# Performance work log

Measured on AMD Instinct MI355X. Metric: run time of the kernel, lower is better.

## Reference

```python
import jax, jax.numpy as jnp
import numpy as np

N_NODES = 100000
N_EDGES = 1600000
DIM = 64
NUM_HEADS = 4
HEAD_DIM = DIM // NUM_HEADS
QK_SCALE = HEAD_DIM ** -0.5
EPS = 1e-16  # matches torch_geometric softmax denominator eps


def setup_inputs() -> dict:
    key = jax.random.key(0)
    k1, k2, k3 = jax.random.split(key, 3)
    x = jax.random.normal(k1, (N_NODES, DIM), dtype=jnp.float32)
    W_qkv = jax.random.normal(k2, (DIM, 3 * DIM), dtype=jnp.float32) * (DIM ** -0.5)
    b_qkv = jnp.zeros((3 * DIM,), dtype=jnp.float32)
    edge_index = jax.random.randint(k3, (2, N_EDGES), 0, N_NODES, dtype=jnp.int64)
    return {"x": x, "W_qkv": W_qkv, "b_qkv": b_qkv, "edge_index": edge_index}


def reference(x, W_qkv, b_qkv, edge_index):
    N = x.shape[0]
    E = edge_index.shape[1]
    # qkv projection: (N, 3, H, d)
    qkv = (x @ W_qkv + b_qkv).reshape(N, 3, NUM_HEADS, HEAD_DIM)
    s = edge_index[0]  # query (source) node per edge
    t = edge_index[1]  # key/value (target) node per edge
    q = qkv[s, 0] * QK_SCALE  # (E, H, d)
    k = qkv[t, 1]             # (E, H, d)
    v = qkv[t, 2]             # (E, H, d)
    compat = jnp.einsum('ehd,ehd->eh', q, k)  # (E, H)
    # segment softmax keyed by source node (numerically stable)
    m = jax.ops.segment_max(compat, s, num_segments=N)          # (N, H)
    ex = jnp.exp(compat - m[s])                                  # (E, H)
    den = jax.ops.segment_sum(ex, s, num_segments=N)             # (N, H)
    attn = ex / (den[s] + EPS)                                   # (E, H)
    # weighted values, flatten heads, scatter-sum back to source nodes
    msg = (v * attn[..., None]).reshape(E, DIM)                  # (E, dim)
    out = jax.ops.segment_sum(msg, s, num_segments=N)            # (N, dim)
    return out
```

## Files before the change

### kernel.cpp

```cpp
#include <hip/hip_runtime.h>

constexpr int N_NODES = 100000;
constexpr int N_EDGES = 1600000;
constexpr int DIM = 64;
constexpr float QK_SCALE = 0.25f;
constexpr float LOG2E = 1.4426950408889634f;
constexpr float EPS = 1e-16f;

constexpr int NBK = (N_NODES + 255) / 256;
constexpr int BCAP = 8192;
constexpr int SC_CHUNK = 4096;
constexpr int SC_BLOCKS = (N_EDGES + SC_CHUNK - 1) / SC_CHUNK;
constexpr int QK_BLOCKS = (N_NODES + 127) / 128;
constexpr int TPAD = 200;

typedef __attribute__((ext_vector_type(8))) short short8;
typedef __attribute__((ext_vector_type(4))) float f32x4;
typedef _Float16 h2 __attribute__((ext_vector_type(2)));

__device__ __forceinline__ unsigned short f32_to_bf16_rne(float f) {
    unsigned int u = __float_as_uint(f);
    u += 0x7fffu + ((u >> 16) & 1u);
    return (unsigned short)(u >> 16);
}
__device__ __forceinline__ h2 as_h2(unsigned int u) { return __builtin_bit_cast(h2, u); }

#if defined(__has_builtin)
#if __has_builtin(__builtin_amdgcn_fdot2)
#define HAVE_FDOT2 1
#endif
#endif
__device__ __forceinline__ float fdot2_acc(h2 a, h2 b, float c) {
#ifdef HAVE_FDOT2
    return __builtin_amdgcn_fdot2(a, b, c, false);
#else
    return fmaf((float)a.x, (float)b.x, fmaf((float)a.y, (float)b.y, c));
#endif
}

__device__ __forceinline__ float qsum4(float p) {
    int a = __builtin_amdgcn_update_dpp(0, __float_as_int(p), 0xB1, 0xF, 0xF, true);
    p += __int_as_float(a);
    int c = __builtin_amdgcn_update_dpp(0, __float_as_int(p), 0x4E, 0xF, 0xF, true);
    p += __int_as_float(c);
    return p;
}

__device__ __forceinline__ int orig_col(int jp) {
    if (jp < 64) return jp;
    const int p = jp - 64;
    const int chunk = p >> 3, w = p & 7;
    return (w < 4) ? (64 + chunk * 4 + w) : (128 + chunk * 4 + (w - 4));
}

__global__ __launch_bounds__(192) void prep_w(const float* __restrict__ W,
                                              const float* __restrict__ b,
                                              unsigned short* __restrict__ Wbt,
                                              float* __restrict__ bb,
                                              int* __restrict__ bcnt) {
    const int jp = threadIdx.x;
    const int k = blockIdx.x;
    const int oc = orig_col(jp);
    const float sc = (jp < 64) ? QK_SCALE * LOG2E : 1.f;
    Wbt[jp * DIM + k] = f32_to_bf16_rne(W[k * 192 + oc] * sc);
    if (k == 0) {
        bb[jp] = b[oc] * sc;
        for (int i = jp; i < NBK; i += 192) bcnt[i] = 0;
    }
}

__global__ __launch_bounds__(512) void proj_scatter(const float* __restrict__ x,
                                                    const unsigned short* __restrict__ Wbt,
                                                    const float* __restrict__ bb,
                                                    unsigned short* __restrict__ qkv_t,
                                                    const int* __restrict__ ei,
                                                    int* __restrict__ bcnt,
                                                    unsigned int* __restrict__ bbuf) {
    __shared__ __align__(16) char smem[128 * TPAD * 2];

    if (blockIdx.x < SC_BLOCKS) {
        unsigned int* stage = (unsigned int*)smem;
        int* h     = (int*)(smem + SC_CHUNK * 4);
        int* lofs  = h + NBK;
        int* gbase = lofs + NBK;
        int* wsum  = gbase + NBK;

        const int tid = threadIdx.x;
        const int lane = tid & 63;
        const int wid = tid >> 6;
        const int e0 = blockIdx.x * SC_CHUNK;
        const int n = min(SC_CHUNK, N_EDGES - e0);
        const int n4 = n >> 2;

        for (int i = tid; i < NBK; i += 512) h[i] = 0;
        __syncthreads();

        const int4* s4p = (const int4*)(ei + e0);
        for (int i = tid; i < n4; i += 512) {
            const int4 s4 = s4p[i];
            atomicAdd(&h[s4.x >> 8], 1);
            atomicAdd(&h[s4.y >> 8], 1);
            atomicAdd(&h[s4.z >> 8], 1);
            atomicAdd(&h[s4.w >> 8], 1);
        }
        __syncthreads();

        const int v = (tid < NBK) ? h[tid] : 0;
        int inc = v;
        #pragma unroll
        for (int d = 1; d < 64; d <<= 1) {
            int u = __shfl_up(inc, d);
            if (lane >= d) inc += u;
        }
        if (lane == 63) wsum[wid] = inc;
        __syncthreads();
        int woff = 0;
        for (int w = 0; w < wid; ++w) woff += wsum[w];
        if (tid < NBK) lofs[tid] = woff + inc - v;
        if (tid < NBK) gbase[tid] = (v > 0) ? atomicAdd(&bcnt[tid], v) : 0;
        __syncthreads();

        for (int i = tid; i < NBK; i += 512) h[i] = 0;
        __syncthreads();

        const int4* t4p = (const int4*)(ei + N_EDGES + e0);
        for (int i = tid; i < n4; i += 512) {
            const int4 s4 = s4p[i];
            const int4 t4 = t4p[i];
            #pragma unroll
            for (int k = 0; k < 4; ++k) {
                const int s = (k == 0) ? s4.x : (k == 1) ? s4.y : (k == 2) ? s4.z : s4.w;
                const int t = (k == 0) ? t4.x : (k == 1) ? t4.y : (k == 2) ? t4.z : t4.w;
                const int bk = s >> 8;
                const int c = atomicAdd(&h[bk], 1);
                stage[lofs[bk] + c] = (unsigned int)t | ((unsigned int)(s & 255) << 17);
            }
        }
        __syncthreads();

        for (int bk = wid; bk < NBK; bk += 8) {
            const int cnt = h[bk];
            const int lo = lofs[bk];
            unsigned int* dst = bbuf + (size_t)bk * BCAP + gbase[bk];
            for (int i = lane; i < cnt; i += 64) dst[i] = stage[lo + i];
        }
    } else {
        unsigned short* tile = (unsigned short*)smem;

        const int tid = threadIdx.x;
        const int lane = tid & 63;
        const int wid = tid >> 6;
        const int nb0 = (blockIdx.x - SC_BLOCKS) * 128;
        const int n0 = nb0 + wid * 16;
        const bool active = n0 < N_NODES;
        const int row = lane & 15;
        const int kg = lane >> 4;

        if (active) {
            const int nidx = min(n0 + row, N_NODES - 1);
            const float* xr = x + (size_t)nidx * DIM + kg * 8;
            short8 a0, a1;
            {
                const float4 u0 = *(const float4*)(xr);
                const float4 u1 = *(const float4*)(xr + 4);
                const float4 u2 = *(const float4*)(xr + 32);
                const float4 u3 = *(const float4*)(xr + 36);
                a0[0] = (short)f32_to_bf16_rne(u0.x); a0[1] = (short)f32_to_bf16_rne(u0.y);
                a0[2] = (short)f32_to_bf16_rne(u0.z); a0[3] = (short)f32_to_bf16_rne(u0.w);
                a0[4] = (short)f32_to_bf16_rne(u1.x); a0[5] = (short)f32_to_bf16_rne(u1.y);
                a0[6] = (short)f32_to_bf16_rne(u1.z); a0[7] = (short)f32_to_bf16_rne(u1.w);
                a1[0] = (short)f32_to_bf16_rne(u2.x); a1[1] = (short)f32_to_bf16_rne(u2.y);
                a1[2] = (short)f32_to_bf16_rne(u2.z); a1[3] = (short)f32_to_bf16_rne(u2.w);
                a1[4] = (short)f32_to_bf16_rne(u3.x); a1[5] = (short)f32_to_bf16_rne(u3.y);
                a1[6] = (short)f32_to_bf16_rne(u3.z); a1[7] = (short)f32_to_bf16_rne(u3.w);
            }

            #pragma unroll
            for (int ct = 0; ct < 12; ++ct) {
                const int c0 = ct * 16;
                const float bias = bb[c0 + row];
                f32x4 acc = {bias, bias, bias, bias};
                const short8 b0 = *(const short8*)(Wbt + (c0 + row) * DIM + kg * 8);
                const short8 b1 = *(const short8*)(Wbt + (c0 + row) * DIM + kg * 8 + 32);
                acc = __builtin_amdgcn_mfma_f32_16x16x32_bf16(a0, b0, acc, 0, 0, 0);
                acc = __builtin_amdgcn_mfma_f32_16x16x32_bf16(a1, b1, acc, 0, 0, 0);

                const int colg = c0 + row;
                #pragma unroll
                for (int r = 0; r < 4; ++r) {
                    const _Float16 hv = (_Float16)acc[r];
                    tile[(wid * 16 + kg * 4 + r) * TPAD + colg] =
                        __builtin_bit_cast(unsigned short, hv);
                }
            }
        }
        __syncthreads();

        for (int i = tid; i < 128 * 24; i += 512) {
            const int r = i / 24, c = i % 24;
            if (nb0 + r < N_NODES) {
                const uint4 val = *(const uint4*)(tile + r * TPAD + c * 8);
                ((uint4*)(qkv_t + (size_t)(nb0 + r) * 192))[c] = val;
            }
        }
    }
}

__global__ __launch_bounds__(512) void csr_build(const int* __restrict__ bcnt,
                                                 const unsigned int* __restrict__ bbuf,
                                                 int* __restrict__ deg,
                                                 int* __restrict__ off,
                                                 int* __restrict__ sorted_t) {
    __shared__ int h[256];
    __shared__ int lofs[256];
    __shared__ int wsum[8];
    __shared__ int sBase;

    const int tid = threadIdx.x;
    const int lane = tid & 63;
    const int wid = tid >> 6;
    const int bk = blockIdx.x;
    const int n = bcnt[bk];

    int pre = 0;
    for (int i = tid; i < bk; i += 512) pre += bcnt[i];
    #pragma unroll
    for (int d = 1; d < 64; d <<= 1) pre += __shfl_xor(pre, d);
    if (lane == 0) wsum[wid] = pre;
    if (tid < 256) h[tid] = 0;
    __syncthreads();
    if (tid == 0) {
        int s = 0;
        #pragma unroll
        for (int w = 0; w < 8; ++w) s += wsum[w];
        sBase = s;
    }
    __syncthreads();

    const unsigned int* p = bbuf + (size_t)bk * BCAP;
    for (int i = tid; i < n; i += 512)
        atomicAdd(&h[p[i] >> 17], 1);
    __syncthreads();

    int v = 0, inc = 0;
    if (tid < 256) {
        v = h[tid];
        inc = v;
        #pragma unroll
        for (int d = 1; d < 64; d <<= 1) {
            int u = __shfl_up(inc, d);
            if (lane >= d) inc += u;
        }
        if (lane == 63) wsum[wid] = inc;
    }
    __syncthreads();
    if (tid < 256) {
        int woff = 0;
        for (int w = 0; w < wid; ++w) woff += wsum[w];
        const int exc = woff + inc - v;
        lofs[tid] = exc;
        const int node = bk * 256 + tid;
        if (node < N_NODES) { deg[node] = v; off[node] = sBase + exc; }
    }
    __syncthreads();

    if (tid < 256) h[tid] = 0;
    __syncthreads();
    int* dstbase = sorted_t + sBase;
    for (int i = tid; i < n; i += 512) {
        const unsigned int e = p[i];
        const int s8 = e >> 17;
        const int c = atomicAdd(&h[s8], 1);
        dstbase[lofs[s8] + c] = (int)(e & 0x1FFFFu);
    }
}

__global__ __launch_bounds__(256) void node_pass(const unsigned short* __restrict__ qkv,
                                                 const int* __restrict__ off,
                                                 const int* __restrict__ deg,
                                                 const int* __restrict__ sorted_t,
                                                 float* __restrict__ out) {
    const int node = blockIdx.x * 4 + (threadIdx.x >> 6);
    const int lane = threadIdx.x & 63;
    if (node >= N_NODES) return;
    const int eg = lane >> 4;
    const int q16 = lane & 15;

    const int o = off[node];
    const int d = deg[node];

    const uint2 qu = *(const uint2*)(qkv + (size_t)node * 192 + q16 * 4);
    const h2 q01 = as_h2(qu.x), q23 = as_h2(qu.y);

    const float M0 = -1e30f, MASKV = -2e30f;
    float m = M0;
    float l = 0.f;
    float4 acc = make_float4(0.f, 0.f, 0.f, 0.f);

    for (int j = 0; j < d; j += 16) {
        const int b0 = j + eg * 4;
        const int dm = d - 1;
        const int t0 = sorted_t[o + min(b0,     dm)];
        const int t1 = sorted_t[o + min(b0 + 1, dm)];
        const int t2 = sorted_t[o + min(b0 + 2, dm)];
        const int t3 = sorted_t[o + min(b0 + 3, dm)];
        const uint4 A0 = *(const uint4*)(qkv + (size_t)t0 * 192 + 64 + q16 * 8);
        const uint4 A1 = *(const uint4*)(qkv + (size_t)t1 * 192 + 64 + q16 * 8);
        const uint4 A2 = *(const uint4*)(qkv + (size_t)t2 * 192 + 64 + q16 * 8);
        const uint4 A3 = *(const uint4*)(qkv + (size_t)t3 * 192 + 64 + q16 * 8);
        float p0 = fdot2_acc(as_h2(A0.y), q23, fdot2_acc(as_h2(A0.x), q01, 0.f));
        float p1 = fdot2_acc(as_h2(A1.y), q23, fdot2_acc(as_h2(A1.x), q01, 0.f));
        float p2 = fdot2_acc(as_h2(A2.y), q23, fdot2_acc(as_h2(A2.x), q01, 0.f));
        float p3 = fdot2_acc(as_h2(A3.y), q23, fdot2_acc(as_h2(A3.x), q01, 0.f));
        p0 = qsum4(p0); p1 = qsum4(p1); p2 = qsum4(p2); p3 = qsum4(p3);
        p0 = (b0     < d) ? p0 : MASKV;
        p1 = (b0 + 1 < d) ? p1 : MASKV;
        p2 = (b0 + 2 < d) ? p2 : MASKV;
        p3 = (b0 + 3 < d) ? p3 : MASKV;
        const float pm = fmaxf(fmaxf(p0, p1), fmaxf(p2, p3));
        if (__any(pm > m)) {
            const float nm = fmaxf(m, pm);
            const float sc = exp2f(m - nm);
            l *= sc;
            acc.x *= sc; acc.y *= sc; acc.z *= sc; acc.w *= sc;
            m = nm;
        }
        const float e0 = exp2f(p0 - m);
        const float e1 = exp2f(p1 - m);
        const float e2 = exp2f(p2 - m);
        const float e3 = exp2f(p3 - m);
        l += (e0 + e1) + (e2 + e3);
        const h2 va0 = as_h2(A0.z), vb0 = as_h2(A0.w);
        const h2 va1 = as_h2(A1.z), vb1 = as_h2(A1.w);
        const h2 va2 = as_h2(A2.z), vb2 = as_h2(A2.w);
        const h2 va3 = as_h2(A3.z), vb3 = as_h2(A3.w);
        acc.x = fmaf(e0, (float)va0.x, fmaf(e1, (float)va1.x,
                fmaf(e2, (float)va2.x, fmaf(e3, (float)va3.x, acc.x))));
        acc.y = fmaf(e0, (float)va0.y, fmaf(e1, (float)va1.y,
                fmaf(e2, (float)va2.y, fmaf(e3, (float)va3.y, acc.y))));
        acc.z = fmaf(e0, (float)vb0.x, fmaf(e1, (float)vb1.x,
                fmaf(e2, (float)vb2.x, fmaf(e3, (float)vb3.x, acc.z))));
        acc.w = fmaf(e0, (float)vb0.y, fmaf(e1, (float)vb1.y,
                fmaf(e2, (float)vb2.y, fmaf(e3, (float)vb3.y, acc.w))));
    }

    float M = fmaxf(m, __shfl_xor(m, 16));
    M = fmaxf(M, __shfl_xor(M, 32));
    const float s = exp2f(m - M);
    l *= s;
    acc.x *= s; acc.y *= s; acc.z *= s; acc.w *= s;

    l += __shfl_xor(l, 16);  l += __shfl_xor(l, 32);
    acc.x += __shfl_xor(acc.x, 16);  acc.x += __shfl_xor(acc.x, 32);
    acc.y += __shfl_xor(acc.y, 16);  acc.y += __shfl_xor(acc.y, 32);
    acc.z += __shfl_xor(acc.z, 16);  acc.z += __shfl_xor(acc.z, 32);
    acc.w += __shfl_xor(acc.w, 16);  acc.w += __shfl_xor(acc.w, 32);

    if (eg == 0) {
        const float inv = 1.f / (l + EPS);
        float4 r = make_float4(acc.x * inv, acc.y * inv, acc.z * inv, acc.w * inv);
        *(float4*)(out + (size_t)node * DIM + q16 * 4) = r;
    }
}

extern "C" void kernel_launch(void* const* d_in, const int* in_sizes, int n_in,
                              void* d_out, int out_size, void* d_ws, size_t ws_size,
                              hipStream_t stream) {
    const float* x = (const float*)d_in[0];
    const float* W = (const float*)d_in[1];
    const float* b = (const float*)d_in[2];
    const int*   ei = (const int*)d_in[3];
    float* out = (float*)d_out;

    unsigned short* qkv_t = (unsigned short*)d_ws;
    unsigned int* bbuf = (unsigned int*)(qkv_t + (size_t)N_NODES * 192);
    int* sorted_t = (int*)(bbuf + (size_t)NBK * BCAP);
    int* deg      = sorted_t + N_EDGES;
    int* off      = deg + N_NODES;
    int* bcnt     = off + N_NODES;
    unsigned short* Wbt = (unsigned short*)(bcnt + NBK);
    float* bb     = (float*)(Wbt + 192 * DIM);

    prep_w<<<64, 192, 0, stream>>>(W, b, Wbt, bb, bcnt);
    proj_scatter<<<SC_BLOCKS + QK_BLOCKS, 512, 0, stream>>>(x, Wbt, bb, qkv_t, ei, bcnt, bbuf);
    csr_build<<<NBK, 512, 0, stream>>>(bcnt, bbuf, deg, off, sorted_t);
    node_pass<<<(N_NODES + 3) / 4, 256, 0, stream>>>(qkv_t, off, deg, sorted_t, out);
}
```

Before: 119.8 us.

## Regroup kernels: fuse weight prep with edge scatter, QKV projection with CSR build

Reassigns work across kernels. Weight preparation now runs as extra blocks alongside the edge bucket scatter. The QKV projection GEMM now runs as extra blocks alongside the CSR build, and bcnt is zeroed with a memset. This takes the projection off the scatter kernel's critical path, lets it overlap with the CSR sort, and removes one kernel boundary. In exchange it adds a memset launch, and the scatter kernel's shared-memory footprint changes.

```diff
diff --git a/kernel.cpp b/kernel.cpp
--- a/kernel.cpp
+++ b/kernel.cpp
@@ -53,96 +53,166 @@
     return (w < 4) ? (64 + chunk * 4 + w) : (128 + chunk * 4 + (w - 4));
 }
 
-__global__ __launch_bounds__(192) void prep_w(const float* __restrict__ W,
-                                              const float* __restrict__ b,
-                                              unsigned short* __restrict__ Wbt,
-                                              float* __restrict__ bb,
-                                              int* __restrict__ bcnt) {
-    const int jp = threadIdx.x;
-    const int k = blockIdx.x;
-    const int oc = orig_col(jp);
-    const float sc = (jp < 64) ? QK_SCALE * LOG2E : 1.f;
-    Wbt[jp * DIM + k] = f32_to_bf16_rne(W[k * 192 + oc] * sc);
-    if (k == 0) {
-        bb[jp] = b[oc] * sc;
-        for (int i = jp; i < NBK; i += 192) bcnt[i] = 0;
-    }
-}
-
-__global__ __launch_bounds__(512) void proj_scatter(const float* __restrict__ x,
-                                                    const unsigned short* __restrict__ Wbt,
-                                                    const float* __restrict__ bb,
-                                                    unsigned short* __restrict__ qkv_t,
-                                                    const int* __restrict__ ei,
+__global__ __launch_bounds__(512) void scatter_prep(const int* __restrict__ ei,
                                                     int* __restrict__ bcnt,
-                                                    unsigned int* __restrict__ bbuf) {
+                                                    unsigned int* __restrict__ bbuf,
+                                                    const float* __restrict__ W,
+                                                    const float* __restrict__ b,
+                                                    unsigned short* __restrict__ Wbt,
+                                                    float* __restrict__ bb) {
+    __shared__ unsigned int stage[SC_CHUNK];
+    __shared__ int h[NBK];
+    __shared__ int lofs[NBK];
+    __shared__ int gbase[NBK];
+    __shared__ int wsum[8];
+
+    if (blockIdx.x >= SC_BLOCKS) {
+        const int k = blockIdx.x - SC_BLOCKS;
+        const int jp = threadIdx.x;
+        if (jp < 192) {
+            const int oc = orig_col(jp);
+            const float sc = (jp < 64) ? QK_SCALE * LOG2E : 1.f;
+            Wbt[jp * DIM + k] = f32_to_bf16_rne(W[k * 192 + oc] * sc);
+            if (k == 0) bb[jp] = b[oc] * sc;
+        }
+        return;
+    }
+
+    const int tid = threadIdx.x;
+    const int lane = tid & 63;
+    const int wid = tid >> 6;
+    const int e0 = blockIdx.x * SC_CHUNK;
+    const int n = min(SC_CHUNK, N_EDGES - e0);
+    const int n4 = n >> 2;
+
+    for (int i = tid; i < NBK; i += 512) h[i] = 0;
+    __syncthreads();
+
+    const int4* s4p = (const int4*)(ei + e0);
+    for (int i = tid; i < n4; i += 512) {
+        const int4 s4 = s4p[i];
+        atomicAdd(&h[s4.x >> 8], 1);
+        atomicAdd(&h[s4.y >> 8], 1);
+        atomicAdd(&h[s4.z >> 8], 1);
+        atomicAdd(&h[s4.w >> 8], 1);
+    }
+    __syncthreads();
+
+    const int v = (tid < NBK) ? h[tid] : 0;
+    int inc = v;
+    #pragma unroll
+    for (int d = 1; d < 64; d <<= 1) {
+        int u = __shfl_up(inc, d);
+        if (lane >= d) inc += u;
+    }
+    if (lane == 63) wsum[wid] = inc;
+    __syncthreads();
+    int woff = 0;
+    for (int w = 0; w < wid; ++w) woff += wsum[w];
+    if (tid < NBK) lofs[tid] = woff + inc - v;
+    if (tid < NBK) gbase[tid] = (v > 0) ? atomicAdd(&bcnt[tid], v) : 0;
+    __syncthreads();
+
+    for (int i = tid; i < NBK; i += 512) h[i] = 0;
+    __syncthreads();
+
+    const int4* t4p = (const int4*)(ei + N_EDGES + e0);
+    for (int i = tid; i < n4; i += 512) {
+        const int4 s4 = s4p[i];
+        const int4 t4 = t4p[i];
+        #pragma unroll
+        for (int k = 0; k < 4; ++k) {
+            const int s = (k == 0) ? s4.x : (k == 1) ? s4.y : (k == 2) ? s4.z : s4.w;
+            const int t = (k == 0) ? t4.x : (k == 1) ? t4.y : (k == 2) ? t4.z : t4.w;
+            const int bk = s >> 8;
+            const int c = atomicAdd(&h[bk], 1);
+            stage[lofs[bk] + c] = (unsigned int)t | ((unsigned int)(s & 255) << 17);
+        }
+    }
+    __syncthreads();
+
+    for (int bk = wid; bk < NBK; bk += 8) {
+        const int cnt = h[bk];
+        const int lo = lofs[bk];
+        unsigned int* dst = bbuf + (size_t)bk * BCAP + gbase[bk];
+        for (int i = lane; i < cnt; i += 64) dst[i] = stage[lo + i];
+    }
+}
+
+__global__ __launch_bounds__(512) void csr_qkv(const int* __restrict__ bcnt,
+                                               const unsigned int* __restrict__ bbuf,
+                                               int* __restrict__ deg,
+                                               int* __restrict__ off,
+                                               int* __restrict__ sorted_t,
+                                               const float* __restrict__ x,
+                                               const unsigned short* __restrict__ Wbt,
+                                               const float* __restrict__ bb,
+                                               unsigned short* __restrict__ qkv_t) {
     __shared__ __align__(16) char smem[128 * TPAD * 2];
 
-    if (blockIdx.x < SC_BLOCKS) {
-        unsigned int* stage = (unsigned int*)smem;
-        int* h     = (int*)(smem + SC_CHUNK * 4);
-        int* lofs  = h + NBK;
-        int* gbase = lofs + NBK;
-        int* wsum  = gbase + NBK;
+    if (blockIdx.x < NBK) {
+        int* h    = (int*)smem;
+        int* lofs = h + 256;
+        int* wsum = lofs + 256;
+        int* sBasep = wsum + 8;
 
         const int tid = threadIdx.x;
         const int lane = tid & 63;
         const int wid = tid >> 6;
-        const int e0 = blockIdx.x * SC_CHUNK;
-        const int n = min(SC_CHUNK, N_EDGES - e0);
-        const int n4 = n >> 2;
-
-        for (int i = tid; i < NBK; i += 512) h[i] = 0;
-        __syncthreads();
-
-        const int4* s4p = (const int4*)(ei + e0);
-        for (int i = tid; i < n4; i += 512) {
-            const int4 s4 = s4p[i];
-            atomicAdd(&h[s4.x >> 8], 1);
-            atomicAdd(&h[s4.y >> 8], 1);
-            atomicAdd(&h[s4.z >> 8], 1);
-            atomicAdd(&h[s4.w >> 8], 1);
-        }
-        __syncthreads();
-
-        const int v = (tid < NBK) ? h[tid] : 0;
-        int inc = v;
+        const int bk = blockIdx.x;
+        const int n = bcnt[bk];
+
+        int pre = 0;
+        for (int i = tid; i < bk; i += 512) pre += bcnt[i];
         #pragma unroll
-        for (int d = 1; d < 64; d <<= 1) {
-            int u = __shfl_up(inc, d);
-            if (lane >= d) inc += u;
-        }
-        if (lane == 63) wsum[wid] = inc;
-        __syncthreads();
-        int woff = 0;
-        for (int w = 0; w < wid; ++w) woff += wsum[w];
-        if (tid < NBK) lofs[tid] = woff + inc - v;
-        if (tid < NBK) gbase[tid] = (v > 0) ? atomicAdd(&bcnt[tid], v) : 0;
-        __syncthreads();
-
-        for (int i = tid; i < NBK; i += 512) h[i] = 0;
-        __syncthreads();
-
-        const int4* t4p = (const int4*)(ei + N_EDGES + e0);
-        for (int i = tid; i < n4; i += 512) {
-            const int4 s4 = s4p[i];
-            const int4 t4 = t4p[i];
+        for (int d = 1; d < 64; d <<= 1) pre += __shfl_xor(pre, d);
+        if (lane == 0) wsum[wid] = pre;
+        if (tid < 256) h[tid] = 0;
+        __syncthreads();
+        if (tid == 0) {
+            int s = 0;
             #pragma unroll
-            for (int k = 0; k < 4; ++k) {
-                const int s = (k == 0) ? s4.x : (k == 1) ? s4.y : (k == 2) ? s4.z : s4.w;
-                const int t = (k == 0) ? t4.x : (k == 1) ? t4.y : (k == 2) ? t4.z : t4.w;
-                const int bk = s >> 8;
-                const int c = atomicAdd(&h[bk], 1);
-                stage[lofs[bk] + c] = (unsigned int)t | ((unsigned int)(s & 255) << 17);
+            for (int w = 0; w < 8; ++w) s += wsum[w];
+            *sBasep = s;
+        }
+        __syncthreads();
+        const int sBase = *sBasep;
+
+        const unsigned int* p = bbuf + (size_t)bk * BCAP;
+        for (int i = tid; i < n; i += 512)
+            atomicAdd(&h[p[i] >> 17], 1);
+        __syncthreads();
+
+        int v = 0, inc = 0;
+        if (tid < 256) {
+            v = h[tid];
+            inc = v;
+            #pragma unroll
+            for (int d = 1; d < 64; d <<= 1) {
+                int u = __shfl_up(inc, d);
+                if (lane >= d) inc += u;
             }
-        }
-        __syncthreads();
-
-        for (int bk = wid; bk < NBK; bk += 8) {
-            const int cnt = h[bk];
-            const int lo = lofs[bk];
-            unsigned int* dst = bbuf + (size_t)bk * BCAP + gbase[bk];
-            for (int i = lane; i < cnt; i += 64) dst[i] = stage[lo + i];
+            if (lane == 63) wsum[wid] = inc;
+        }
+        __syncthreads();
+        if (tid < 256) {
+            int woff = 0;
+            for (int w = 0; w < wid; ++w) woff += wsum[w];
+            const int exc = woff + inc - v;
+            lofs[tid] = exc;
+            const int node = bk * 256 + tid;
+            if (node < N_NODES) { deg[node] = v; off[node] = sBase + exc; }
+        }
+        __syncthreads();
+
+        if (tid < 256) h[tid] = 0;
+        __syncthreads();
+        int* dstbase = sorted_t + sBase;
+        for (int i = tid; i < n; i += 512) {
+            const unsigned int e = p[i];
+            const int s8 = e >> 17;
+            const int c = atomicAdd(&h[s8], 1);
+            dstbase[lofs[s8] + c] = (int)(e & 0x1FFFFu);
         }
     } else {
         unsigned short* tile = (unsigned short*)smem;
@@ -150,7 +220,7 @@
         const int tid = threadIdx.x;
         const int lane = tid & 63;
         const int wid = tid >> 6;
-        const int nb0 = (blockIdx.x - SC_BLOCKS) * 128;
+        const int nb0 = (blockIdx.x - NBK) * 128;
         const int n0 = nb0 + wid * 16;
         const bool active = n0 < N_NODES;
         const int row = lane & 15;
@@ -203,75 +273,6 @@
                 ((uint4*)(qkv_t + (size_t)(nb0 + r) * 192))[c] = val;
             }
         }
-    }
-}
-
-__global__ __launch_bounds__(512) void csr_build(const int* __restrict__ bcnt,
-                                                 const unsigned int* __restrict__ bbuf,
-                                                 int* __restrict__ deg,
-                                                 int* __restrict__ off,
-                                                 int* __restrict__ sorted_t) {
-    __shared__ int h[256];
-    __shared__ int lofs[256];
-    __shared__ int wsum[8];
-    __shared__ int sBase;
-
-    const int tid = threadIdx.x;
-    const int lane = tid & 63;
-    const int wid = tid >> 6;
-    const int bk = blockIdx.x;
-    const int n = bcnt[bk];
-
-    int pre = 0;
-    for (int i = tid; i < bk; i += 512) pre += bcnt[i];
-    #pragma unroll
-    for (int d = 1; d < 64; d <<= 1) pre += __shfl_xor(pre, d);
-    if (lane == 0) wsum[wid] = pre;
-    if (tid < 256) h[tid] = 0;
-    __syncthreads();
-    if (tid == 0) {
-        int s = 0;
-        #pragma unroll
-        for (int w = 0; w < 8; ++w) s += wsum[w];
-        sBase = s;
-    }
-    __syncthreads();
-
-    const unsigned int* p = bbuf + (size_t)bk * BCAP;
-    for (int i = tid; i < n; i += 512)
-        atomicAdd(&h[p[i] >> 17], 1);
-    __syncthreads();
-
-    int v = 0, inc = 0;
-    if (tid < 256) {
-        v = h[tid];
-        inc = v;
-        #pragma unroll
-        for (int d = 1; d < 64; d <<= 1) {
-            int u = __shfl_up(inc, d);
-            if (lane >= d) inc += u;
-        }
-        if (lane == 63) wsum[wid] = inc;
-    }
-    __syncthreads();
-    if (tid < 256) {
-        int woff = 0;
-        for (int w = 0; w < wid; ++w) woff += wsum[w];
-        const int exc = woff + inc - v;
-        lofs[tid] = exc;
-        const int node = bk * 256 + tid;
-        if (node < N_NODES) { deg[node] = v; off[node] = sBase + exc; }
-    }
-    __syncthreads();
-
-    if (tid < 256) h[tid] = 0;
-    __syncthreads();
-    int* dstbase = sorted_t + sBase;
-    for (int i = tid; i < n; i += 512) {
-        const unsigned int e = p[i];
-        const int s8 = e >> 17;
-        const int c = atomicAdd(&h[s8], 1);
-        dstbase[lofs[s8] + c] = (int)(e & 0x1FFFFu);
     }
 }
 
@@ -381,8 +382,9 @@
     unsigned short* Wbt = (unsigned short*)(bcnt + NBK);
     float* bb     = (float*)(Wbt + 192 * DIM);
 
-    prep_w<<<64, 192, 0, stream>>>(W, b, Wbt, bb, bcnt);
-    proj_scatter<<<SC_BLOCKS + QK_BLOCKS, 512, 0, stream>>>(x, Wbt, bb, qkv_t, ei, bcnt, bbuf);
-    csr_build<<<NBK, 512, 0, stream>>>(bcnt, bbuf, deg, off, sorted_t);
+    hipMemsetAsync(bcnt, 0, NBK * sizeof(int), stream);
+    scatter_prep<<<SC_BLOCKS + 64, 512, 0, stream>>>(ei, bcnt, bbuf, W, b, Wbt, bb);
+    csr_qkv<<<NBK + QK_BLOCKS, 512, 0, stream>>>(bcnt, bbuf, deg, off, sorted_t,
+                                                 x, Wbt, bb, qkv_t);
     node_pass<<<(N_NODES + 3) / 4, 256, 0, stream>>>(qkv_t, off, deg, sorted_t, out);
 }
```

New measurement: 130.2 us. +8.6%, slower.
